# Optimization experiments

Measured on AMD Instinct MI355X. Metric: run time of the kernel, lower is better.

## Reference

```python
import jax, jax.numpy as jnp
import numpy as np

N = 32          # LPC order
T = 1048576     # number of frames
EPS = 1e-05


def setup_inputs() -> dict:
    key = jax.random.key(0)
    # Diagonally dominant autocorrelation: r0 = 1, sum_k |r_k| <= 0.9 < r0,
    # so the Toeplitz system is positive definite and E stays > 0.
    lags = jax.random.uniform(key, (1, N, T), minval=-1.0, maxval=1.0) * (0.9 / N)
    r0 = jnp.ones((1, 1, T), dtype=jnp.float32)
    pAC = jnp.concatenate([r0, lags.astype(jnp.float32)], axis=1)  # [1, N+1, T]
    return {"pAC": pAC}


def _levinson(pAC):
    ac = pAC[0]                       # [N+1, T]
    E = ac[0]                         # [T]
    lp = jnp.zeros((N, ac.shape[-1]), dtype=pAC.dtype)  # [N, T]
    for i in range(N):                # unrolled over fixed order N (static)
        if i > 0:
            # sum_j lp[j] * ac[i - j], j = 0..i-1  ->  ac[1:i+1] reversed
            acc = jnp.sum(lp[:i] * ac[1:i + 1][::-1], axis=0)
            ki = (ac[i + 1] + acc) / E
        else:
            ki = ac[1] / E
        c = jnp.clip(1.0 - ki * ki, EPS, None)
        E = E * c
        if i > 0:
            # pTmp[j] = lp[j] - ki * lp[i-1-j], from OLD lp (separate buffer)
            lp = lp.at[:i].set(lp[:i] - ki * lp[:i][::-1])
        lp = lp.at[i].set(-ki)
    return lp[None]                   # [1, N, T]


def reference(pAC):
    return _levinson(pAC)
```

## Files before the change

kernel.cpp:

```cpp
#include <hip/hip_runtime.h>

#define LPC_N 32
#define LPC_EPS 1e-5f

typedef float f2 __attribute__((ext_vector_type(2)));

__device__ __forceinline__ f2 rcp2(f2 v) {
    f2 r;
    r.x = __builtin_amdgcn_rcpf(v.x);
    r.y = __builtin_amdgcn_rcpf(v.y);
    return r;
}

__global__ __launch_bounds__(256) void levinson_kernel(
    const float* __restrict__ pAC,
    float* __restrict__ out,
    int T)
{
    int p = blockIdx.x * blockDim.x + threadIdx.x;
    int TP = T >> 1;
    if (p >= TP) return;

    f2 ac[LPC_N + 1];
#pragma unroll
    for (int i = 0; i <= LPC_N; ++i) {
        ac[i] = *(const f2*)(pAC + (size_t)i * T + 2 * (size_t)p);
    }

    f2 lp[LPC_N];
    f2 E = ac[0];

#pragma unroll
    for (int i = 0; i < LPC_N; ++i) {
        f2 invE = rcp2(E);

        f2 s0 = ac[i + 1];
        f2 s1 = {0.0f, 0.0f};
#pragma unroll
        for (int j = 0; j + 1 < i; j += 2) {
            s0 += lp[j]     * ac[i - j];
            s1 += lp[j + 1] * ac[i - j - 1];
        }
        if (i & 1) {
            s0 += lp[i - 1] * ac[1];
        }
        f2 acc = s0 + s1;

        f2 ki = acc * invE;
        f2 c  = {1.0f, 1.0f};
        c -= ki * ki;
        c.x = fmaxf(c.x, LPC_EPS);
        c.y = fmaxf(c.y, LPC_EPS);
        E *= c;

#pragma unroll
        for (int j = 0; j < i - 1 - j; ++j) {
            f2 a = lp[j];
            f2 b = lp[i - 1 - j];
            lp[j]         = a - ki * b;
            lp[i - 1 - j] = b - ki * a;
        }
        if (i & 1) {
            int m = (i - 1) >> 1;
            lp[m] = lp[m] - ki * lp[m];
        }
        lp[i] = -ki;
    }

#pragma unroll
    for (int i = 0; i < LPC_N; ++i) {
        *(f2*)(out + (size_t)i * T + 2 * (size_t)p) = lp[i];
    }
}

extern "C" void kernel_launch(void* const* d_in, const int* in_sizes, int n_in,
                              void* d_out, int out_size, void* d_ws, size_t ws_size,
                              hipStream_t stream)
{
    const float* pAC = (const float*)d_in[0];
    float* out = (float*)d_out;
    int T = in_sizes[0] / (LPC_N + 1);

    int TP = T >> 1;
    int block = 256;
    int grid = (TP + block - 1) / block;
    levinson_kernel<<<grid, block, 0, stream>>>(pAC, out, T);
}
```

Before: 240.7 us.

## Spill upper autocorrelation lags to LDS to raise occupancy, use nontemporal stores

Only the first 14 autocorrelation lags stay in registers. The remaining 19 lags go into per-wave shared memory and are read back through an accessor. Launch bounds now request a minimum of 4 blocks per SM, and the outputs are written with nontemporal stores. The aim is to cut VGPR pressure so more waves are resident to hide memory latency, at the cost of LDS reads inside the inner dot-product loop.

```diff
diff --git a/kernel.cpp b/kernel.cpp
--- a/kernel.cpp
+++ b/kernel.cpp
@@ -2,6 +2,8 @@
 
 #define LPC_N 32
 #define LPC_EPS 1e-5f
+#define NREG 14
+#define NLDS (LPC_N + 1 - NREG)
 
 typedef float f2 __attribute__((ext_vector_type(2)));
 
@@ -12,20 +14,36 @@
     return r;
 }
 
-__global__ __launch_bounds__(256) void levinson_kernel(
+__global__ __launch_bounds__(256, 4) void levinson_kernel(
     const float* __restrict__ pAC,
     float* __restrict__ out,
     int T)
 {
-    int p = blockIdx.x * blockDim.x + threadIdx.x;
-    int TP = T >> 1;
+    __shared__ f2 smem[4 * NLDS * 64];
+
+    const int tid  = threadIdx.x;
+    const int lane = tid & 63;
+    const int wv   = tid >> 6;
+    const int p    = blockIdx.x * blockDim.x + tid;
+    const int TP   = T >> 1;
     if (p >= TP) return;
 
-    f2 ac[LPC_N + 1];
+    f2* wbuf = smem + wv * (NLDS * 64);
+
 #pragma unroll
-    for (int i = 0; i <= LPC_N; ++i) {
-        ac[i] = *(const f2*)(pAC + (size_t)i * T + 2 * (size_t)p);
+    for (int k = 0; k < NLDS; ++k) {
+        f2 v = *(const f2*)(pAC + (size_t)(NREG + k) * T + 2 * (size_t)p);
+        wbuf[k * 64 + lane] = v;
     }
+
+    f2 ac[NREG];
+#pragma unroll
+    for (int k = 0; k < NREG; ++k)
+        ac[k] = *(const f2*)(pAC + (size_t)k * T + 2 * (size_t)p);
+
+    auto AC = [&](int m) -> f2 {
+        return (m < NREG) ? ac[m] : wbuf[(m - NREG) * 64 + lane];
+    };
 
     f2 lp[LPC_N];
     f2 E = ac[0];
@@ -34,12 +52,12 @@
     for (int i = 0; i < LPC_N; ++i) {
         f2 invE = rcp2(E);
 
-        f2 s0 = ac[i + 1];
+        f2 s0 = AC(i + 1);
         f2 s1 = {0.0f, 0.0f};
 #pragma unroll
         for (int j = 0; j + 1 < i; j += 2) {
-            s0 += lp[j]     * ac[i - j];
-            s1 += lp[j + 1] * ac[i - j - 1];
+            s0 += lp[j]     * AC(i - j);
+            s1 += lp[j + 1] * AC(i - j - 1);
         }
         if (i & 1) {
             s0 += lp[i - 1] * ac[1];
@@ -69,7 +87,7 @@
 
 #pragma unroll
     for (int i = 0; i < LPC_N; ++i) {
-        *(f2*)(out + (size_t)i * T + 2 * (size_t)p) = lp[i];
+        __builtin_nontemporal_store(lp[i], (f2*)(out + (size_t)i * T + 2 * (size_t)p));
     }
 }
 
```

New measurement: 261.3 us. 8.5% more time.
